# Kernel optimization log

Measured on AMD Instinct MI355X. Metric: run time of the kernel, lower is better.

## Reference

```python
import jax, jax.numpy as jnp
import numpy as np

NEG_SLOPE = 0.2


def _gat_layer(x, src, dst, W, att_s, att_d, bias):
    # x: [N, F_in]; W: [F_in, H*C]; att_s/att_d: [H, C]; bias: [H*C]
    N = x.shape[0]
    H, C = att_s.shape
    h = (x @ W).reshape(N, H, C)                      # projected features [N,H,C]
    a_src = jnp.einsum('nhc,hc->nh', h, att_s)        # [N,H] per-node src logits
    a_dst = jnp.einsum('nhc,hc->nh', h, att_d)        # [N,H]
    e = a_src[src] + a_dst[dst]                       # [E,H] edge logits
    e = jnp.where(e > 0, e, NEG_SLOPE * e)            # leaky_relu
    # scatter-softmax over incoming edges of each destination node
    m = jax.ops.segment_max(e, dst, num_segments=N)   # [N,H]
    ex = jnp.exp(e - m[dst])                          # [E,H]
    denom = jax.ops.segment_sum(ex, dst, num_segments=N)  # [N,H]
    alpha = ex / denom[dst]                           # [E,H]
    # scatter-add aggregation of weighted source features
    msg = h[src] * alpha[:, :, None]                  # [E,H,C]
    out = jax.ops.segment_sum(msg, dst, num_segments=N)   # [N,H,C]
    return out.reshape(N, H * C) + bias


def _with_self_loops(edge_index, N):
    loop = jnp.arange(N, dtype=edge_index.dtype)
    src = jnp.concatenate([edge_index[0], loop])
    dst = jnp.concatenate([edge_index[1], loop])
    return src, dst


def setup_inputs() -> dict:
    key = jax.random.key(0)
    ks = jax.random.split(key, 10)
    N, E = 50000, 800000
    F_in, C1, H1, F_out = 128, 64, 4, 128
    x = jax.random.normal(ks[0], (N, F_in), dtype=jnp.float32)
    edge_index = jax.random.randint(ks[1], (2, E), 0, N, dtype=jnp.int64)
    s1 = 1.0 / np.sqrt(F_in)
    W1 = jax.random.normal(ks[2], (F_in, H1 * C1), dtype=jnp.float32) * s1
    att_src1 = jax.random.normal(ks[3], (H1, C1), dtype=jnp.float32) * 0.1
    att_dst1 = jax.random.normal(ks[4], (H1, C1), dtype=jnp.float32) * 0.1
    bias1 = jnp.zeros((H1 * C1,), dtype=jnp.float32)
    s2 = 1.0 / np.sqrt(H1 * C1)
    W2 = jax.random.normal(ks[5], (H1 * C1, F_out), dtype=jnp.float32) * s2
    att_src2 = jax.random.normal(ks[6], (1, F_out), dtype=jnp.float32) * 0.1
    att_dst2 = jax.random.normal(ks[7], (1, F_out), dtype=jnp.float32) * 0.1
    bias2 = jnp.zeros((F_out,), dtype=jnp.float32)
    return {"x": x, "edge_index": edge_index,
            "W1": W1, "att_src1": att_src1, "att_dst1": att_dst1, "bias1": bias1,
            "W2": W2, "att_src2": att_src2, "att_dst2": att_dst2, "bias2": bias2}


def reference(x, edge_index, W1, att_src1, att_dst1, bias1,
              W2, att_src2, att_dst2, bias2):
    N = x.shape[0]
    src, dst = _with_self_loops(edge_index, N)
    h1 = _gat_layer(x, src, dst, W1, att_src1, att_dst1, bias1)
    h1 = jax.nn.elu(h1)
    out = _gat_layer(h1, src, dst, W2, att_src2, att_dst2, bias2)
    return out
```

## Files before the change

### kernel.cpp

```cpp
#include <hip/hip_runtime.h>

#define NN 50000
#define NE 800000

constexpr int H1 = 4, F1 = 128, HC1 = 256;
constexpr int HC2 = 128;

typedef unsigned short u16;
typedef unsigned int u32;
typedef __attribute__((ext_vector_type(8))) short bf16x8;
typedef __attribute__((ext_vector_type(4))) float f32x4;

__device__ __forceinline__ float bf2f(u16 h) {
    return __uint_as_float(((u32)h) << 16);
}
__device__ __forceinline__ u16 f2bf(float f) {
    u32 u = __float_as_uint(f);
    u32 r = (u + 0x7fffu + ((u >> 16) & 1u)) >> 16;
    return (u16)r;
}

__device__ __forceinline__ int ld_edge(const int* e32, const long long* e64, int is64, long long idx) {
    return is64 ? (int)e64[idx] : e32[idx];
}

__global__ __launch_bounds__(256) void k_cvt(const float* __restrict__ in, u16* __restrict__ out, int n8) {
    int i = blockIdx.x * 256 + threadIdx.x;
    if (i >= n8) return;
    const float4* p = (const float4*)in + (size_t)i * 2;
    float4 a = p[0], b = p[1];
    ushort4 o0, o1;
    o0.x = f2bf(a.x); o0.y = f2bf(a.y); o0.z = f2bf(a.z); o0.w = f2bf(a.w);
    o1.x = f2bf(b.x); o1.y = f2bf(b.y); o1.z = f2bf(b.z); o1.w = f2bf(b.w);
    ((ushort4*)out)[(size_t)i * 2] = o0;
    ((ushort4*)out)[(size_t)i * 2 + 1] = o1;
}

__global__ void k_zero_detect(int* __restrict__ p, const int* __restrict__ e32, int* __restrict__ flag) {
    int i = blockIdx.x * blockDim.x + threadIdx.x;
    if (i < NN) p[i] = 0;
    if (i == 0) {
        int z = 1;
        for (int t = 0; t < 16; t++)
            if (e32[2 * t + 1] != 0) z = 0;
        *flag = z;
    }
}

__global__ void k_count(const int* __restrict__ e32, const long long* __restrict__ e64,
                        const int* __restrict__ flag, int* __restrict__ deg) {
    int e = blockIdx.x * blockDim.x + threadIdx.x;
    if (e >= NE) return;
    int is64 = *flag;
    int dst = ld_edge(e32, e64, is64, (long long)NE + e);
    atomicAdd(&deg[dst], 1);
}

__global__ __launch_bounds__(256) void k_part(const int* __restrict__ deg, int* __restrict__ bsum) {
    int i = blockIdx.x * 256 + threadIdx.x;
    int v = (i < NN) ? deg[i] : 0;
    #pragma unroll
    for (int off = 1; off < 64; off <<= 1) v += __shfl_xor(v, off);
    __shared__ int ws[4];
    if ((threadIdx.x & 63) == 0) ws[threadIdx.x >> 6] = v;
    __syncthreads();
    if (threadIdx.x == 0) bsum[blockIdx.x] = ws[0] + ws[1] + ws[2] + ws[3];
}

__global__ __launch_bounds__(256) void k_scanb(const int* __restrict__ bsum, int* __restrict__ boff,
                                               int* __restrict__ row_ptr, int NB) {
    const int tid = threadIdx.x;
    const int lane = tid & 63, wv = tid >> 6;
    int v = (tid < NB) ? bsum[tid] : 0;
    int x = v;
    #pragma unroll
    for (int off = 1; off < 64; off <<= 1) {
        int t = __shfl_up(x, off);
        if (lane >= off) x += t;
    }
    __shared__ int wsum[4], woff[4];
    if (lane == 63) wsum[wv] = x;
    __syncthreads();
    if (tid == 0) {
        int run = 0;
        #pragma unroll
        for (int j = 0; j < 4; j++) { woff[j] = run; run += wsum[j]; }
        row_ptr[NN] = run;
    }
    __syncthreads();
    if (tid < NB) boff[tid] = x - v + woff[wv];
}

__global__ __launch_bounds__(256) void k_addb(const int* __restrict__ deg, const int* __restrict__ boff,
                                              int* __restrict__ row_ptr, int* __restrict__ cursor) {
    const int tid = threadIdx.x;
    const int lane = tid & 63, wv = tid >> 6;
    int i = blockIdx.x * 256 + tid;
    int v = (i < NN) ? deg[i] : 0;
    int x = v;
    #pragma unroll
    for (int off = 1; off < 64; off <<= 1) {
        int t = __shfl_up(x, off);
        if (lane >= off) x += t;
    }
    __shared__ int wsum[4], woff[4];
    if (lane == 63) wsum[wv] = x;
    __syncthreads();
    if (tid == 0) {
        int run = 0;
        #pragma unroll
        for (int j = 0; j < 4; j++) { woff[j] = run; run += wsum[j]; }
    }
    __syncthreads();
    int excl = x - v + woff[wv] + boff[blockIdx.x];
    if (i < NN) { row_ptr[i] = excl; cursor[i] = excl; }
}

__global__ void k_fill(const int* __restrict__ e32, const long long* __restrict__ e64,
                       const int* __restrict__ flag, int* __restrict__ cursor, int* __restrict__ col) {
    int e = blockIdx.x * blockDim.x + threadIdx.x;
    if (e >= NE) return;
    int is64 = *flag;
    int src = ld_edge(e32, e64, is64, e);
    int dst = ld_edge(e32, e64, is64, (long long)NE + e);
    int pos = atomicAdd(&cursor[dst], 1);
    col[pos] = src;
}

template <int K, int N>
__global__ __launch_bounds__(256) void k_prepw(const float* __restrict__ W, u16* __restrict__ Wp) {
    constexpr int LGN = (N == 256) ? 8 : 7;
    int o = blockIdx.x * 256 + threadIdx.x;
    if (o >= K * N) return;
    int j = o & 7;
    int lk = (o >> 3) & 3;
    int nn = (o >> 5) & (N - 1);
    int kc = o >> (5 + LGN);
    int k = kc * 32 + lk * 8 + j;
    Wp[o] = f2bf(W[(size_t)k * N + nn]);
}

template <int K, int NOUT, int HEADS, int TPB>
__global__ __launch_bounds__(TPB) void k_gemm_mfma(
    const u16* __restrict__ Ab, const u16* __restrict__ Wp,
    const float* __restrict__ atts, const float* __restrict__ attd,
    u16* __restrict__ Hout, float* __restrict__ as_out, float* __restrict__ ad_out, int M)
{
    constexpr int BM = 64, BK = 32;
    constexpr int NK = K / BK;
    constexpr int C = NOUT / HEADS;
    constexpr int LDA = 40;
    __shared__ __align__(16) u16 As[2][BM * LDA];
    __shared__ float red_s[BM * HEADS];
    __shared__ float red_d[BM * HEADS];

    const int tid = threadIdx.x;
    const int w = tid >> 6;
    const int l = tid & 63;
    const int l15 = l & 15, lk = l >> 4;
    const int row0 = blockIdx.x * BM;
    const int col0 = w * 64;

    for (int i = tid; i < BM * HEADS; i += TPB) { red_s[i] = 0.f; red_d[i] = 0.f; }

    f32x4 acc[4][4];
    #pragma unroll
    for (int rt = 0; rt < 4; rt++)
        #pragma unroll
        for (int nt = 0; nt < 4; nt++)
            acc[rt][nt] = (f32x4){0.f, 0.f, 0.f, 0.f};

    auto stage = [&](int kc, int b) {
        #pragma unroll
        for (int i = tid; i < BM * 4; i += TPB) {
            int r = i >> 2, c = (i & 3) * 8;
            int gr = row0 + r;
            bf16x8 v = {0, 0, 0, 0, 0, 0, 0, 0};
            if (gr < M) v = *(const bf16x8*)(Ab + (size_t)gr * K + kc * BK + c);
            *(bf16x8*)&As[b][r * LDA + c] = v;
        }
    };
    auto loadB = [&](int kc, bf16x8* bf) {
        #pragma unroll
        for (int nt = 0; nt < 4; nt++)
            bf[nt] = *(const bf16x8*)(Wp + (((size_t)kc * NOUT + col0 + nt * 16 + l15) * 4 + lk) * 8);
    };

    bf16x8 bcur[4];
    loadB(0, bcur);
    stage(0, 0);
    for (int kc = 0; kc < NK; ++kc) {
        __syncthreads();
        bf16x8 afr[4];
        #pragma unroll
        for (int rt = 0; rt < 4; rt++)
            afr[rt] = *(const bf16x8*)&As[kc & 1][(rt * 16 + l15) * LDA + lk * 8];
        bf16x8 bnext[4];
        if (kc + 1 < NK) {
            loadB(kc + 1, bnext);
            stage(kc + 1, (kc + 1) & 1);
        }
        #pragma unroll
        for (int rt = 0; rt < 4; rt++)
            #pragma unroll
            for (int nt = 0; nt < 4; nt++)
                acc[rt][nt] = __builtin_amdgcn_mfma_f32_16x16x32_bf16(afr[rt], bcur[nt], acc[rt][nt], 0, 0, 0);
        if (kc + 1 < NK) {
            #pragma unroll
            for (int nt = 0; nt < 4; nt++) bcur[nt] = bnext[nt];
        }
    }

    #pragma unroll
    for (int rt = 0; rt < 4; rt++) {
        #pragma unroll
        for (int t = 0; t < 4; t++) {
            int gr = row0 + rt * 16 + lk * 4 + t;
            if (gr < M) {
                #pragma unroll
                for (int nt = 0; nt < 4; nt++)
                    Hout[(size_t)gr * NOUT + col0 + nt * 16 + l15] = f2bf(acc[rt][nt][t]);
            }
        }
    }

    float avs[4], avd[4];
    #pragma unroll
    for (int nt = 0; nt < 4; nt++) {
        int gc = col0 + nt * 16 + l15;
        avs[nt] = atts[gc];
        avd[nt] = attd[gc];
    }
    const int headw = col0 / C;
    #pragma unroll
    for (int rt = 0; rt < 4; rt++) {
        #pragma unroll
        for (int t = 0; t < 4; t++) {
            float ps = 0.f, pd = 0.f;
            #pragma unroll
            for (int nt = 0; nt < 4; nt++) {
                ps = fmaf(acc[rt][nt][t], avs[nt], ps);
                pd = fmaf(acc[rt][nt][t], avd[nt], pd);
            }
            ps += __shfl_xor(ps, 1); ps += __shfl_xor(ps, 2);
            ps += __shfl_xor(ps, 4); ps += __shfl_xor(ps, 8);
            pd += __shfl_xor(pd, 1); pd += __shfl_xor(pd, 2);
            pd += __shfl_xor(pd, 4); pd += __shfl_xor(pd, 8);
            if (l15 == 0) {
                int row = rt * 16 + lk * 4 + t;
                atomicAdd(&red_s[row * HEADS + headw], ps);
                atomicAdd(&red_d[row * HEADS + headw], pd);
            }
        }
    }
    __syncthreads();
    for (int i = tid; i < BM * HEADS; i += TPB) {
        int gr = row0 + i / HEADS;
        if (gr < M) {
            as_out[(size_t)gr * HEADS + i % HEADS] = red_s[i];
            ad_out[(size_t)gr * HEADS + i % HEADS] = red_d[i];
        }
    }
}

__global__ __launch_bounds__(256) void k_agg1(
    const int* __restrict__ row_ptr, const int* __restrict__ col,
    const u16* __restrict__ Hb, const float* __restrict__ as_, const float* __restrict__ ad_,
    const float* __restrict__ bias, u16* __restrict__ outp)
{
    __shared__ int    s_src[4][64];
    __shared__ float4 s_p[4][64];
    int n = blockIdx.x * 4 + (threadIdx.x >> 6);
    if (n >= NN) return;
    const int lane = threadIdx.x & 63;
    const int wv = threadIdx.x >> 6;
    const int head = lane >> 4;
    float4 ad4 = *(const float4*)(ad_ + (size_t)n * 4);
    int beg = row_ptr[n];
    int cnt = row_ptr[n + 1] - beg + 1;
    float4 sp = make_float4(0.f, 0.f, 0.f, 0.f);
    float ax = 0.f, ay = 0.f, az = 0.f, aw = 0.f;
    for (int c = 0; c < cnt; c += 64) {
        int idx = c + lane;
        int srcl = n;
        float4 p4 = make_float4(0.f, 0.f, 0.f, 0.f);
        if (idx < cnt) {
            srcl = (idx == 0) ? n : col[beg + idx - 1];
            float4 a4 = *(const float4*)(as_ + (size_t)srcl * 4);
            float e;
            e = a4.x + ad4.x; e = e > 0.f ? e : 0.2f * e; p4.x = __expf(e);
            e = a4.y + ad4.y; e = e > 0.f ? e : 0.2f * e; p4.y = __expf(e);
            e = a4.z + ad4.z; e = e > 0.f ? e : 0.2f * e; p4.z = __expf(e);
            e = a4.w + ad4.w; e = e > 0.f ? e : 0.2f * e; p4.w = __expf(e);
        }
        sp.x += p4.x; sp.y += p4.y; sp.z += p4.z; sp.w += p4.w;
        s_src[wv][lane] = srcl;
        s_p[wv][lane] = p4;
        int jmax = min(64, cnt - c);
        #pragma unroll 4
        for (int j = 0; j < jmax; ++j) {
            int srcj = s_src[wv][j];
            float pj = ((const float*)&s_p[wv][j])[head];
            ushort4 hv = *(const ushort4*)(Hb + (size_t)srcj * HC1 + lane * 4);
            ax = fmaf(pj, bf2f(hv.x), ax);
            ay = fmaf(pj, bf2f(hv.y), ay);
            az = fmaf(pj, bf2f(hv.z), az);
            aw = fmaf(pj, bf2f(hv.w), aw);
        }
    }
    #pragma unroll
    for (int off = 1; off < 64; off <<= 1) {
        sp.x += __shfl_xor(sp.x, off);
        sp.y += __shfl_xor(sp.y, off);
        sp.z += __shfl_xor(sp.z, off);
        sp.w += __shfl_xor(sp.w, off);
    }
    float s = head < 2 ? (head == 0 ? sp.x : sp.y) : (head == 2 ? sp.z : sp.w);
    float inv = 1.f / s;
    float4 bv = *(const float4*)(bias + lane * 4);
    float4 o;
    o.x = ax * inv + bv.x;
    o.y = ay * inv + bv.y;
    o.z = az * inv + bv.z;
    o.w = aw * inv + bv.w;
    o.x = o.x > 0.f ? o.x : __expf(o.x) - 1.f;
    o.y = o.y > 0.f ? o.y : __expf(o.y) - 1.f;
    o.z = o.z > 0.f ? o.z : __expf(o.z) - 1.f;
    o.w = o.w > 0.f ? o.w : __expf(o.w) - 1.f;
    ushort4 ob;
    ob.x = f2bf(o.x); ob.y = f2bf(o.y); ob.z = f2bf(o.z); ob.w = f2bf(o.w);
    *(ushort4*)(outp + (size_t)n * HC1 + lane * 4) = ob;
}

__global__ __launch_bounds__(256) void k_agg2(
    const int* __restrict__ row_ptr, const int* __restrict__ col,
    const u16* __restrict__ Hb, const float* __restrict__ as_, const float* __restrict__ ad_,
    const float* __restrict__ bias, float* __restrict__ outp)
{
    __shared__ int   s_src[4][64];
    __shared__ float s_p[4][64];
    int n = blockIdx.x * 4 + (threadIdx.x >> 6);
    if (n >= NN) return;
    const int lane = threadIdx.x & 63;
    const int wv = threadIdx.x >> 6;
    float ad0 = ad_[n];
    int beg = row_ptr[n];
    int cnt = row_ptr[n + 1] - beg + 1;
    float sp = 0.f;
    float ax = 0.f, ay = 0.f;
    for (int c = 0; c < cnt; c += 64) {
        int idx = c + lane;
        int srcl = n;
        float p = 0.f;
        if (idx < cnt) {
            srcl = (idx == 0) ? n : col[beg + idx - 1];
            float e = as_[srcl] + ad0;
            e = e > 0.f ? e : 0.2f * e;
            p = __expf(e);
        }
        sp += p;
        s_src[wv][lane] = srcl;
        s_p[wv][lane] = p;
        int jmax = min(64, cnt - c);
        #pragma unroll 4
        for (int j = 0; j < jmax; ++j) {
            int srcj = s_src[wv][j];
            float pj = s_p[wv][j];
            ushort2 hv = *(const ushort2*)(Hb + (size_t)srcj * HC2 + lane * 2);
            ax = fmaf(pj, bf2f(hv.x), ax);
            ay = fmaf(pj, bf2f(hv.y), ay);
        }
    }
    #pragma unroll
    for (int off = 1; off < 64; off <<= 1) sp += __shfl_xor(sp, off);
    float inv = 1.f / sp;
    float2 bv = *(const float2*)(bias + lane * 2);
    float2 o = make_float2(ax * inv + bv.x, ay * inv + bv.y);
    *(float2*)(outp + (size_t)n * HC2 + lane * 2) = o;
}

extern "C" void kernel_launch(void* const* d_in, const int* in_sizes, int n_in,
                              void* d_out, int out_size, void* d_ws, size_t ws_size,
                              hipStream_t stream) {
    const float* x   = (const float*)d_in[0];
    const int*       e32 = (const int*)d_in[1];
    const long long* e64 = (const long long*)d_in[1];
    const float* W1  = (const float*)d_in[2];
    const float* as1w = (const float*)d_in[3];
    const float* ad1w = (const float*)d_in[4];
    const float* b1  = (const float*)d_in[5];
    const float* W2  = (const float*)d_in[6];
    const float* as2w = (const float*)d_in[7];
    const float* ad2w = (const float*)d_in[8];
    const float* b2  = (const float*)d_in[9];
    float* out = (float*)d_out;

    char* w = (char*)d_ws;
    auto carve = [&](size_t bytes) -> void* {
        void* p = (void*)w;
        w += (bytes + 255) & ~(size_t)255;
        return p;
    };
    int*   flag    = (int*)carve(4);
    int*   row_ptr = (int*)carve((NN + 1) * sizeof(int));
    int*   cursor  = (int*)carve(NN * sizeof(int));
    int*   col     = (int*)carve(NE * sizeof(int));
    int*   bsum    = (int*)carve(256 * sizeof(int));
    int*   boff    = (int*)carve(256 * sizeof(int));
    float* as1     = (float*)carve((size_t)NN * H1 * sizeof(float));
    float* ad1     = (float*)carve((size_t)NN * H1 * sizeof(float));
    float* as2     = (float*)carve((size_t)NN * sizeof(float));
    float* ad2     = (float*)carve((size_t)NN * sizeof(float));
    u16*   xb      = (u16*)carve((size_t)NN * F1 * sizeof(u16));
    u16*   h1b     = (u16*)carve((size_t)NN * HC1 * sizeof(u16));
    u16*   h2in    = (u16*)carve((size_t)NN * HC1 * sizeof(u16));
    u16*   h2b     = (u16*)carve((size_t)NN * HC2 * sizeof(u16));
    u16*   wp1     = (u16*)carve((size_t)F1 * HC1 * sizeof(u16));
    u16*   wp2     = (u16*)carve((size_t)HC1 * HC2 * sizeof(u16));

    const int TPB = 256;
    const int gN  = (NN + TPB - 1) / TPB;
    const int gE  = (NE + TPB - 1) / TPB;
    const int gM  = (NN + 63) / 64;
    const int gAgg = (NN + 3) / 4;

    k_cvt<<<(NN * F1 / 8 + 255) / 256, 256, 0, stream>>>(x, xb, NN * F1 / 8);
    k_prepw<F1, HC1><<<F1 * HC1 / 256, 256, 0, stream>>>(W1, wp1);
    k_prepw<HC1, HC2><<<HC1 * HC2 / 256, 256, 0, stream>>>(W2, wp2);

    k_zero_detect<<<gN, TPB, 0, stream>>>(cursor, e32, flag);
    k_count<<<gE, TPB, 0, stream>>>(e32, e64, flag, cursor);
    k_part<<<gN, TPB, 0, stream>>>(cursor, bsum);
    k_scanb<<<1, 256, 0, stream>>>(bsum, boff, row_ptr, gN);
    k_addb<<<gN, TPB, 0, stream>>>(cursor, boff, row_ptr, cursor);
    k_fill<<<gE, TPB, 0, stream>>>(e32, e64, flag, cursor, col);

    k_gemm_mfma<F1, HC1, H1, 256><<<gM, 256, 0, stream>>>(xb, wp1, as1w, ad1w, h1b, as1, ad1, NN);
    k_agg1<<<gAgg, TPB, 0, stream>>>(row_ptr, col, h1b, as1, ad1, b1, h2in);

    k_gemm_mfma<HC1, HC2, 1, 128><<<gM, 128, 0, stream>>>(h2in, wp2, as2w, ad2w, h2b, as2, ad2, NN);
    k_agg2<<<gAgg, TPB, 0, stream>>>(row_ptr, col, h2b, as2, ad2, b2, out);
}
```

Before: 240.5 us.

## Fold attention vectors into weights, fuse prep kernels, store self-loops in CSR

```diff
diff --git a/kernel.cpp b/kernel.cpp
--- a/kernel.cpp
+++ b/kernel.cpp
@@ -24,21 +24,64 @@
     return is64 ? (int)e64[idx] : e32[idx];
 }
 
-__global__ __launch_bounds__(256) void k_cvt(const float* __restrict__ in, u16* __restrict__ out, int n8) {
-    int i = blockIdx.x * 256 + threadIdx.x;
-    if (i >= n8) return;
-    const float4* p = (const float4*)in + (size_t)i * 2;
-    float4 a = p[0], b = p[1];
-    ushort4 o0, o1;
-    o0.x = f2bf(a.x); o0.y = f2bf(a.y); o0.z = f2bf(a.z); o0.w = f2bf(a.w);
-    o1.x = f2bf(b.x); o1.y = f2bf(b.y); o1.z = f2bf(b.z); o1.w = f2bf(b.w);
-    ((ushort4*)out)[(size_t)i * 2] = o0;
-    ((ushort4*)out)[(size_t)i * 2 + 1] = o1;
+__global__ __launch_bounds__(256) void k_prep(
+    const float* __restrict__ x, const float* __restrict__ W1, const float* __restrict__ W2,
+    const float* __restrict__ as1w, const float* __restrict__ ad1w,
+    const float* __restrict__ as2w, const float* __restrict__ ad2w,
+    u16* __restrict__ xb, u16* __restrict__ wp1, u16* __restrict__ wp2,
+    float* __restrict__ wa1, float* __restrict__ wa2)
+{
+    const int b = blockIdx.x, tid = threadIdx.x;
+    if (b < 3125) {
+        int i = b * 256 + tid;
+        const float4* p = (const float4*)x + (size_t)i * 2;
+        float4 a = p[0], c = p[1];
+        ushort4 o0, o1;
+        o0.x = f2bf(a.x); o0.y = f2bf(a.y); o0.z = f2bf(a.z); o0.w = f2bf(a.w);
+        o1.x = f2bf(c.x); o1.y = f2bf(c.y); o1.z = f2bf(c.z); o1.w = f2bf(c.w);
+        ((ushort4*)xb)[(size_t)i * 2] = o0;
+        ((ushort4*)xb)[(size_t)i * 2 + 1] = o1;
+    } else if (b < 3253) {
+        int o = (b - 3125) * 256 + tid;
+        int j = o & 7, lk = (o >> 3) & 3, nn = (o >> 5) & 255, kc = o >> 13;
+        int k = kc * 32 + lk * 8 + j;
+        wp1[o] = f2bf(W1[(size_t)k * HC1 + nn]);
+    } else if (b < 3381) {
+        int o = (b - 3253) * 256 + tid;
+        int j = o & 7, lk = (o >> 3) & 3, nn = (o >> 5) & 127, kc = o >> 12;
+        int k = kc * 32 + lk * 8 + j;
+        wp2[o] = f2bf(W2[(size_t)k * HC2 + nn]);
+    } else {
+        #pragma unroll
+        for (int pp = 0; pp < 2; pp++) {
+            int p = tid + pp * 256;
+            int k = p >> 2, h = p & 3;
+            float s = 0.f, d = 0.f;
+            for (int c = 0; c < 64; c++) {
+                float wv = W1[(size_t)k * HC1 + h * 64 + c];
+                s = fmaf(wv, as1w[h * 64 + c], s);
+                d = fmaf(wv, ad1w[h * 64 + c], d);
+            }
+            wa1[h * 128 + k] = s;
+            wa1[(4 + h) * 128 + k] = d;
+        }
+        {
+            int k = tid;
+            float s = 0.f, d = 0.f;
+            for (int c = 0; c < 128; c++) {
+                float wv = W2[(size_t)k * HC2 + c];
+                s = fmaf(wv, as2w[c], s);
+                d = fmaf(wv, ad2w[c], d);
+            }
+            wa2[k * 2] = s;
+            wa2[k * 2 + 1] = d;
+        }
+    }
 }
 
 __global__ void k_zero_detect(int* __restrict__ p, const int* __restrict__ e32, int* __restrict__ flag) {
     int i = blockIdx.x * blockDim.x + threadIdx.x;
-    if (i < NN) p[i] = 0;
+    if (i < NN) p[i] = 1;
     if (i == 0) {
         int z = 1;
         for (int t = 0; t < 16; t++)
@@ -92,7 +135,8 @@
 }
 
 __global__ __launch_bounds__(256) void k_addb(const int* __restrict__ deg, const int* __restrict__ boff,
-                                              int* __restrict__ row_ptr, int* __restrict__ cursor) {
+                                              int* __restrict__ row_ptr, int* __restrict__ cursor,
+                                              int* __restrict__ col) {
     const int tid = threadIdx.x;
     const int lane = tid & 63, wv = tid >> 6;
     int i = blockIdx.x * 256 + tid;
@@ -113,7 +157,11 @@
     }
     __syncthreads();
     int excl = x - v + woff[wv] + boff[blockIdx.x];
-    if (i < NN) { row_ptr[i] = excl; cursor[i] = excl; }
+    if (i < NN) {
+        row_ptr[i] = excl;
+        cursor[i] = excl + 1;
+        col[excl] = i;
+    }
 }
 
 __global__ void k_fill(const int* __restrict__ e32, const long long* __restrict__ e64,
@@ -127,32 +175,14 @@
     col[pos] = src;
 }
 
-template <int K, int N>
-__global__ __launch_bounds__(256) void k_prepw(const float* __restrict__ W, u16* __restrict__ Wp) {
-    constexpr int LGN = (N == 256) ? 8 : 7;
-    int o = blockIdx.x * 256 + threadIdx.x;
-    if (o >= K * N) return;
-    int j = o & 7;
-    int lk = (o >> 3) & 3;
-    int nn = (o >> 5) & (N - 1);
-    int kc = o >> (5 + LGN);
-    int k = kc * 32 + lk * 8 + j;
-    Wp[o] = f2bf(W[(size_t)k * N + nn]);
-}
-
-template <int K, int NOUT, int HEADS, int TPB>
+template <int K, int NOUT, int TPB>
 __global__ __launch_bounds__(TPB) void k_gemm_mfma(
-    const u16* __restrict__ Ab, const u16* __restrict__ Wp,
-    const float* __restrict__ atts, const float* __restrict__ attd,
-    u16* __restrict__ Hout, float* __restrict__ as_out, float* __restrict__ ad_out, int M)
+    const u16* __restrict__ Ab, const u16* __restrict__ Wp, u16* __restrict__ Hout, int M)
 {
     constexpr int BM = 64, BK = 32;
     constexpr int NK = K / BK;
-    constexpr int C = NOUT / HEADS;
     constexpr int LDA = 40;
     __shared__ __align__(16) u16 As[2][BM * LDA];
-    __shared__ float red_s[BM * HEADS];
-    __shared__ float red_d[BM * HEADS];
 
     const int tid = threadIdx.x;
     const int w = tid >> 6;
@@ -160,8 +190,6 @@
     const int l15 = l & 15, lk = l >> 4;
     const int row0 = blockIdx.x * BM;
     const int col0 = w * 64;
-
-    for (int i = tid; i < BM * HEADS; i += TPB) { red_s[i] = 0.f; red_d[i] = 0.f; }
 
     f32x4 acc[4][4];
     #pragma unroll
@@ -223,69 +251,57 @@
             }
         }
     }
-
-    float avs[4], avd[4];
-    #pragma unroll
-    for (int nt = 0; nt < 4; nt++) {
-        int gc = col0 + nt * 16 + l15;
-        avs[nt] = atts[gc];
-        avd[nt] = attd[gc];
-    }
-    const int headw = col0 / C;
-    #pragma unroll
-    for (int rt = 0; rt < 4; rt++) {
-        #pragma unroll
-        for (int t = 0; t < 4; t++) {
-            float ps = 0.f, pd = 0.f;
-            #pragma unroll
-            for (int nt = 0; nt < 4; nt++) {
-                ps = fmaf(acc[rt][nt][t], avs[nt], ps);
-                pd = fmaf(acc[rt][nt][t], avd[nt], pd);
-            }
-            ps += __shfl_xor(ps, 1); ps += __shfl_xor(ps, 2);
-            ps += __shfl_xor(ps, 4); ps += __shfl_xor(ps, 8);
-            pd += __shfl_xor(pd, 1); pd += __shfl_xor(pd, 2);
-            pd += __shfl_xor(pd, 4); pd += __shfl_xor(pd, 8);
-            if (l15 == 0) {
-                int row = rt * 16 + lk * 4 + t;
-                atomicAdd(&red_s[row * HEADS + headw], ps);
-                atomicAdd(&red_d[row * HEADS + headw], pd);
-            }
-        }
-    }
-    __syncthreads();
-    for (int i = tid; i < BM * HEADS; i += TPB) {
-        int gr = row0 + i / HEADS;
-        if (gr < M) {
-            as_out[(size_t)gr * HEADS + i % HEADS] = red_s[i];
-            ad_out[(size_t)gr * HEADS + i % HEADS] = red_d[i];
-        }
+}
+
+__global__ __launch_bounds__(256) void k_logits1(
+    const u16* __restrict__ xb, const float* __restrict__ wa1,
+    float* __restrict__ as1, float* __restrict__ ad1)
+{
+    __shared__ float wsm[8 * 128];
+    for (int i = threadIdx.x; i < 1024; i += 256) wsm[i] = wa1[i];
+    __syncthreads();
+    int n = blockIdx.x * 4 + (threadIdx.x >> 6);
+    int l = threadIdx.x & 63;
+    u32 xx = *(const u32*)(xb + (size_t)n * F1 + l * 2);
+    float x0 = bf2f((u16)(xx & 0xffff)), x1 = bf2f((u16)(xx >> 16));
+    float a[8];
+    #pragma unroll
+    for (int j = 0; j < 8; j++)
+        a[j] = x0 * wsm[j * 128 + l * 2] + x1 * wsm[j * 128 + l * 2 + 1];
+    #pragma unroll
+    for (int off = 1; off < 64; off <<= 1) {
+        #pragma unroll
+        for (int j = 0; j < 8; j++) a[j] += __shfl_xor(a[j], off);
+    }
+    if (l == 0) {
+        *(float4*)(as1 + (size_t)n * 4) = make_float4(a[0], a[1], a[2], a[3]);
+        *(float4*)(ad1 + (size_t)n * 4) = make_float4(a[4], a[5], a[6], a[7]);
     }
 }
 
 __global__ __launch_bounds__(256) void k_agg1(
     const int* __restrict__ row_ptr, const int* __restrict__ col,
     const u16* __restrict__ Hb, const float* __restrict__ as_, const float* __restrict__ ad_,
-    const float* __restrict__ bias, u16* __restrict__ outp)
+    const float* __restrict__ bias, const float* __restrict__ wa2,
+    u16* __restrict__ outp, float* __restrict__ as2, float* __restrict__ ad2)
 {
     __shared__ int    s_src[4][64];
     __shared__ float4 s_p[4][64];
     int n = blockIdx.x * 4 + (threadIdx.x >> 6);
-    if (n >= NN) return;
     const int lane = threadIdx.x & 63;
     const int wv = threadIdx.x >> 6;
     const int head = lane >> 4;
     float4 ad4 = *(const float4*)(ad_ + (size_t)n * 4);
     int beg = row_ptr[n];
-    int cnt = row_ptr[n + 1] - beg + 1;
+    int cnt = row_ptr[n + 1] - beg;
     float4 sp = make_float4(0.f, 0.f, 0.f, 0.f);
     float ax = 0.f, ay = 0.f, az = 0.f, aw = 0.f;
     for (int c = 0; c < cnt; c += 64) {
         int idx = c + lane;
-        int srcl = n;
+        int srcl = 0;
         float4 p4 = make_float4(0.f, 0.f, 0.f, 0.f);
         if (idx < cnt) {
-            srcl = (idx == 0) ? n : col[beg + idx - 1];
+            srcl = __builtin_nontemporal_load(col + beg + idx);
             float4 a4 = *(const float4*)(as_ + (size_t)srcl * 4);
             float e;
             e = a4.x + ad4.x; e = e > 0.f ? e : 0.2f * e; p4.x = __expf(e);
@@ -330,6 +346,17 @@
     ushort4 ob;
     ob.x = f2bf(o.x); ob.y = f2bf(o.y); ob.z = f2bf(o.z); ob.w = f2bf(o.w);
     *(ushort4*)(outp + (size_t)n * HC1 + lane * 4) = ob;
+
+    float4 wA = *(const float4*)(wa2 + lane * 8);
+    float4 wB = *(const float4*)(wa2 + lane * 8 + 4);
+    float s2 = o.x * wA.x + o.y * wA.z + o.z * wB.x + o.w * wB.z;
+    float d2 = o.x * wA.y + o.y * wA.w + o.z * wB.y + o.w * wB.w;
+    #pragma unroll
+    for (int off = 1; off < 64; off <<= 1) {
+        s2 += __shfl_xor(s2, off);
+        d2 += __shfl_xor(d2, off);
+    }
+    if (lane == 0) { as2[n] = s2; ad2[n] = d2; }
 }
 
 __global__ __launch_bounds__(256) void k_agg2(
@@ -340,20 +367,19 @@
     __shared__ int   s_src[4][64];
     __shared__ float s_p[4][64];
     int n = blockIdx.x * 4 + (threadIdx.x >> 6);
-    if (n >= NN) return;
     const int lane = threadIdx.x & 63;
     const int wv = threadIdx.x >> 6;
     float ad0 = ad_[n];
     int beg = row_ptr[n];
-    int cnt = row_ptr[n + 1] - beg + 1;
+    int cnt = row_ptr[n + 1] - beg;
     float sp = 0.f;
     float ax = 0.f, ay = 0.f;
     for (int c = 0; c < cnt; c += 64) {
         int idx = c + lane;
-        int srcl = n;
+        int srcl = 0;
         float p = 0.f;
         if (idx < cnt) {
-            srcl = (idx == 0) ? n : col[beg + idx - 1];
+            srcl = __builtin_nontemporal_load(col + beg + idx);
             float e = as_[srcl] + ad0;
             e = e > 0.f ? e : 0.2f * e;
             p = __expf(e);
@@ -404,7 +430,7 @@
     int*   flag    = (int*)carve(4);
     int*   row_ptr = (int*)carve((NN + 1) * sizeof(int));
     int*   cursor  = (int*)carve(NN * sizeof(int));
-    int*   col     = (int*)carve(NE * sizeof(int));
+    int*   col     = (int*)carve((NE + NN) * sizeof(int));
     int*   bsum    = (int*)carve(256 * sizeof(int));
     int*   boff    = (int*)carve(256 * sizeof(int));
     float* as1     = (float*)carve((size_t)NN * H1 * sizeof(float));
@@ -417,27 +443,28 @@
     u16*   h2b     = (u16*)carve((size_t)NN * HC2 * sizeof(u16));
     u16*   wp1     = (u16*)carve((size_t)F1 * HC1 * sizeof(u16));
     u16*   wp2     = (u16*)carve((size_t)HC1 * HC2 * sizeof(u16));
+    float* wa1     = (float*)carve(8 * 128 * sizeof(float));
+    float* wa2     = (float*)carve(256 * 2 * sizeof(float));
 
     const int TPB = 256;
     const int gN  = (NN + TPB - 1) / TPB;
     const int gE  = (NE + TPB - 1) / TPB;
     const int gM  = (NN + 63) / 64;
-    const int gAgg = (NN + 3) / 4;
-
-    k_cvt<<<(NN * F1 / 8 + 255) / 256, 256, 0, stream>>>(x, xb, NN * F1 / 8);
-    k_prepw<F1, HC1><<<F1 * HC1 / 256, 256, 0, stream>>>(W1, wp1);
-    k_prepw<HC1, HC2><<<HC1 * HC2 / 256, 256, 0, stream>>>(W2, wp2);
+    const int gAgg = NN / 4;
+
+    k_prep<<<3382, 256, 0, stream>>>(x, W1, W2, as1w, ad1w, as2w, ad2w, xb, wp1, wp2, wa1, wa2);
 
     k_zero_detect<<<gN, TPB, 0, stream>>>(cursor, e32, flag);
     k_count<<<gE, TPB, 0, stream>>>(e32, e64, flag, cursor);
     k_part<<<gN, TPB, 0, stream>>>(cursor, bsum);
     k_scanb<<<1, 256, 0, stream>>>(bsum, boff, row_ptr, gN);
-    k_addb<<<gN, TPB, 0, stream>>>(cursor, boff, row_ptr, cursor);
+    k_addb<<<gN, TPB, 0, stream>>>(cursor, boff, row_ptr, cursor, col);
     k_fill<<<gE, TPB, 0, stream>>>(e32, e64, flag, cursor, col);
 
-    k_gemm_mfma<F1, HC1, H1, 256><<<gM, 256, 0, stream>>>(xb, wp1, as1w, ad1w, h1b, as1, ad1, NN);
-    k_agg1<<<gAgg, TPB, 0, stream>>>(row_ptr, col, h1b, as1, ad1, b1, h2in);
-
-    k_gemm_mfma<HC1, HC2, 1, 128><<<gM, 128, 0, stream>>>(h2in, wp2, as2w, ad2w, h2b, as2, ad2, NN);
+    k_gemm_mfma<F1, HC1, 256><<<gM, 256, 0, stream>>>(xb, wp1, h1b, NN);
+    k_logits1<<<gAgg, 256, 0, stream>>>(xb, wa1, as1, ad1);
+    k_agg1<<<gAgg, TPB, 0, stream>>>(row_ptr, col, h1b, as1, ad1, b1, wa2, h2in, as2, ad2);
+
+    k_gemm_mfma<HC1, HC2, 128><<<gM, 128, 0, stream>>>(h2in, wp2, h2b, NN);
     k_agg2<<<gAgg, TPB, 0, stream>>>(row_ptr, col, h2b, as2, ad2, b2, out);
 }
```

Result: slower. 276.0 us (+14.8%).
